# Kernel optimization log

Hardware: AMD Instinct MI355X
Metric: run time of the kernel (lower is better)

The kernel has to match this reference:

```python
import jax, jax.numpy as jnp
import numpy as np

THRESHOLD = 0.3
NEG_BIG = -2.0 ** 32  # matches tf -2**32 causal mask constant


def setup_inputs() -> dict:
    key = jax.random.key(0)
    kq, kt, kv = jax.random.split(key, 3)
    B, S, D = 16, 2048, 128
    Q = jax.random.normal(kq, (B, S, D), dtype=jnp.float32)
    T = jax.random.normal(kt, (B, S, D), dtype=jnp.float32)
    V = jax.random.normal(kv, (B, S, D), dtype=jnp.float32)
    return {"Q": Q, "T": T, "V": V}


def reference(Q, T, V):
    # scores: [B, S, S]
    A = jnp.einsum('bqd,bkd->bqk', Q, T)
    # Faithful to tf.where(A>thr, A, -2**32 * cast(A>thr)):
    # the false branch evaluates to 0 (mask is 0 there), NOT -2**32.
    A = jnp.where(A > THRESHOLD, A, jnp.zeros((), A.dtype))
    S = Q.shape[1]
    causal = jnp.triu(jnp.ones((S, S), dtype=bool), k=1)  # strictly upper = masked
    A = A + jnp.where(causal, jnp.asarray(NEG_BIG, A.dtype), jnp.zeros((), A.dtype))
    d_k = jnp.asarray(Q.shape[-1], A.dtype)
    A = A / jnp.sqrt(d_k)
    y = jax.nn.softmax(A, axis=-1)
    return jnp.einsum('bqk,bkd->bqd', y, V)
```

## Files before the change

kernel.cpp:

```cpp
#include <hip/hip_runtime.h>
#include <hip/hip_bf16.h>


#define S_LEN 2048
#define D_DIM 128
#define THRESH 0.3f
#define SCALE 0.08838834764831845f

typedef __bf16 bf16x8 __attribute__((ext_vector_type(8)));
typedef __bf16 bf16x4 __attribute__((ext_vector_type(4)));
typedef float f32x4 __attribute__((ext_vector_type(4)));

#define GLD16(g, l)                                                         \
    __builtin_amdgcn_global_load_lds(                                       \
        (const __attribute__((address_space(1))) unsigned int*)(g),         \
        (__attribute__((address_space(3))) unsigned int*)(l), 16, 0, 0)

__global__ void prep_kernel(const float* __restrict__ V, const float* __restrict__ T,
                            __bf16* __restrict__ Vt, __bf16* __restrict__ Tb) {
    __shared__ float tile[64][65];
    int bid = blockIdx.x;
    int tid = threadIdx.x;
    int b  = bid >> 6;
    int t2 = bid & 63;

    {
        int flat = tid * 16;
        int r = flat >> 7, cc = flat & 127;
        const float* p = T + ((size_t)b * S_LEN + t2 * 32 + r) * D_DIM + cc;
        __bf16* q = Tb + ((size_t)b * S_LEN + t2 * 32 + r) * D_DIM + cc;
        bf16x8 w0, w1;
        f32x4 a0 = *(const f32x4*)p,       a1 = *(const f32x4*)(p + 4);
        f32x4 a2 = *(const f32x4*)(p + 8), a3 = *(const f32x4*)(p + 12);
        #pragma unroll
        for (int j = 0; j < 4; ++j) {
            w0[j] = (__bf16)a0[j]; w0[4 + j] = (__bf16)a1[j];
            w1[j] = (__bf16)a2[j]; w1[4 + j] = (__bf16)a3[j];
        }
        *(bf16x8*)q = w0;
        *(bf16x8*)(q + 8) = w1;
    }

    int s0 = (t2 >> 1) * 64;
    int d0 = (t2 & 1) * 64;
    #pragma unroll
    for (int it = 0; it < 2; ++it) {
        int row = it * 32 + (tid >> 3);
        int c   = (tid & 7) * 8;
        const float* p = V + ((size_t)b * S_LEN + s0 + row) * D_DIM + d0 + c;
        *(f32x4*)(&tile[row][c])     = *(const f32x4*)p;
        *(f32x4*)(&tile[row][c + 4]) = *(const f32x4*)(p + 4);
    }
    __syncthreads();
    #pragma unroll
    for (int it = 0; it < 2; ++it) {
        int dr = it * 32 + (tid >> 3);
        int c  = (tid & 7) * 8;
        bf16x8 w;
        #pragma unroll
        for (int j = 0; j < 8; ++j) w[j] = (__bf16)tile[c + j][dr];
        *(bf16x8*)(Vt + ((size_t)b * D_DIM + d0 + dr) * S_LEN + s0 + c) = w;
    }
}

__global__ __launch_bounds__(256, 2)
void fa_kernel(const float* __restrict__ Q, const __bf16* __restrict__ Tb,
               const __bf16* __restrict__ Vt, float* __restrict__ O,
               float* __restrict__ pO, float* __restrict__ pL) {
    __shared__ __align__(16) unsigned char smem[73728];

    const int bid = blockIdx.x;
    const int b   = bid & 15;
    const int pi  = (bid >> 4) & 15;
    const int c   = bid >> 8;
    const int qtH = 31 - pi;
    const int L   = pi + 1;

    const int tid  = threadIdx.x;
    const int lane = tid & 63;
    const int wv   = tid >> 6;
    const int col  = lane & 15;
    const int quad = lane >> 4;

    unsigned char* Pb = smem + 65536;
    float* Lxf = (float*)(smem + 65536);

    const __bf16* TbB = Tb + (size_t)b * (S_LEN * D_DIM);
    const __bf16* VtB = Vt + (size_t)b * (D_DIM * S_LEN);

    int toff[4], voff[4];
    #pragma unroll
    for (int i = 0; i < 4; ++i) {
        int trw = wv * 16 + i * 4 + (lane >> 4);
        toff[i] = trw * 128 + (((lane & 15) ^ (trw & 7)) << 3);
        int drw = wv * 32 + i * 8 + (lane >> 3);
        voff[i] = drw * 2048 + (((lane & 7) ^ (drw & 7)) << 3);
    }

    auto issueTile = [&](int k0, int buf) {
        const __bf16* ts = TbB + (size_t)k0 * D_DIM;
        const __bf16* vs = VtB + k0;
        unsigned char* lt = smem + buf * 16384 + wv * 4096;
        unsigned char* lv = smem + 32768 + buf * 16384 + wv * 4096;
        #pragma unroll
        for (int i = 0; i < 4; ++i) GLD16(ts + toff[i], lt + i * 1024);
        #pragma unroll
        for (int i = 0; i < 4; ++i) GLD16(vs + voff[i], lv + i * 1024);
    };

    bf16x8 qf[4][4];
    auto loadQ = [&](int jq) {
        #pragma unroll
        for (int t = 0; t < 4; ++t) {
            const float* qptr = Q + ((size_t)b * S_LEN + jq * 64 + 16 * t + col) * D_DIM + quad * 8;
            #pragma unroll
            for (int kk = 0; kk < 4; ++kk) {
                f32x4 a = *(const f32x4*)(qptr + kk * 32);
                f32x4 d = *(const f32x4*)(qptr + kk * 32 + 4);
                #pragma unroll
                for (int j = 0; j < 4; ++j) { qf[t][kk][j] = (__bf16)a[j]; qf[t][kk][4 + j] = (__bf16)d[j]; }
            }
        }
    };

    f32x4 oacc[4][2];
    float lsum[4];
    float lfull[4][4];

    auto computeTile = [&](int buf, bool diag) {
        unsigned char* Tt = smem + buf * 16384;
        unsigned char* Vl = smem + 32768 + buf * 16384;

        f32x4 sacc[4];
        #pragma unroll
        for (int t = 0; t < 4; ++t) sacc[t] = {0.f, 0.f, 0.f, 0.f};
        __builtin_amdgcn_s_setprio(1);
        #pragma unroll
        for (int kk = 0; kk < 4; ++kk) {
            int trow = wv * 16 + col;
            bf16x8 tf = *(const bf16x8*)(Tt + trow * 256 + ((kk * 64 + quad * 16) ^ ((trow & 7) << 4)));
            #pragma unroll
            for (int t = 0; t < 4; ++t)
                sacc[t] = __builtin_amdgcn_mfma_f32_16x16x32_bf16(tf, qf[t][kk], sacc[t], 0, 0, 0);
        }
        __builtin_amdgcn_s_setprio(0);

        float p[4][4];
        #pragma unroll
        for (int t = 0; t < 4; ++t)
            #pragma unroll
            for (int r = 0; r < 4; ++r) {
                float s = sacc[t][r];
                float e = __expf(s * SCALE);
                p[t][r] = (s > THRESH) ? e : 1.0f;
            }
        if (diag) {
            #pragma unroll
            for (int t = 0; t < 4; ++t)
                #pragma unroll
                for (int r = 0; r < 4; ++r)
                    if (wv * 16 + quad * 4 + r > 16 * t + col) p[t][r] = 0.0f;
        }
        #pragma unroll
        for (int t = 0; t < 4; ++t)
            lsum[t] += (p[t][0] + p[t][1]) + (p[t][2] + p[t][3]);

        #pragma unroll
        for (int t = 0; t < 4; ++t) {
            int row = 16 * t + col;
            bf16x4 w = {(__bf16)p[t][0], (__bf16)p[t][1], (__bf16)p[t][2], (__bf16)p[t][3]};
            *(bf16x4*)(Pb + row * 128 + ((32 * wv + 8 * quad) ^ ((row & 7) << 4))) = w;
        }
        asm volatile("s_waitcnt lgkmcnt(0)" ::: "memory");
        __builtin_amdgcn_s_barrier();

        __builtin_amdgcn_s_setprio(1);
        #pragma unroll
        for (int kb = 0; kb < 2; ++kb) {
            bf16x8 pf[4];
            #pragma unroll
            for (int t = 0; t < 4; ++t) {
                int prow = 16 * t + col;
                pf[t] = *(const bf16x8*)(Pb + prow * 128 + ((kb * 64 + quad * 16) ^ ((prow & 7) << 4)));
            }
            #pragma unroll
            for (int dn = 0; dn < 2; ++dn) {
                int vrow = 32 * wv + 16 * dn + col;
                bf16x8 vf = *(const bf16x8*)(Vl + vrow * 128 + ((kb * 64 + quad * 16) ^ ((vrow & 7) << 4)));
                #pragma unroll
                for (int t = 0; t < 4; ++t)
                    oacc[t][dn] = __builtin_amdgcn_mfma_f32_16x16x32_bf16(pf[t], vf, oacc[t][dn], 0, 0, 0);
            }
        }
        __builtin_amdgcn_s_setprio(0);
    };

    auto runSeg = [&](int jq, int k0t, int nt) {
        loadQ(jq);
        #pragma unroll
        for (int t = 0; t < 4; ++t) {
            oacc[t][0] = {0.f, 0.f, 0.f, 0.f};
            oacc[t][1] = {0.f, 0.f, 0.f, 0.f};
            lsum[t] = 0.f;
        }
        issueTile(k0t * 64, 0);
        for (int s = 0; s < nt; ++s) {
            if (s + 1 < nt) {
                issueTile((k0t + s + 1) * 64, (s + 1) & 1);
                asm volatile("s_waitcnt vmcnt(8)" ::: "memory");
            } else {
                asm volatile("s_waitcnt vmcnt(0)" ::: "memory");
            }
            __builtin_amdgcn_s_barrier();
            computeTile(s & 1, k0t + s == jq);
            __builtin_amdgcn_s_barrier();
        }
    };

    auto finishSeg = [&]() {
        #pragma unroll
        for (int t = 0; t < 4; ++t) {
            float lw = lsum[t];
            lw += __shfl_xor(lw, 16);
            lw += __shfl_xor(lw, 32);
            if (quad == 0) Lxf[wv * 64 + 16 * t + col] = lw;
        }
        __syncthreads();
        #pragma unroll
        for (int t = 0; t < 4; ++t)
            #pragma unroll
            for (int r = 0; r < 4; ++r) {
                int q = 16 * t + quad * 4 + r;
                lfull[t][r] = (Lxf[q] + Lxf[64 + q]) + (Lxf[128 + q] + Lxf[192 + q]);
            }
        __syncthreads();
    };

    auto storeO = [&](int jq) {
        float* optr = O + ((size_t)b * S_LEN + jq * 64) * D_DIM;
        #pragma unroll
        for (int t = 0; t < 4; ++t)
            #pragma unroll
            for (int r = 0; r < 4; ++r) {
                float inv = 1.0f / lfull[t][r];
                #pragma unroll
                for (int dn = 0; dn < 2; ++dn)
                    optr[(16 * t + quad * 4 + r) * D_DIM + 32 * wv + 16 * dn + col] = oacc[t][dn][r] * inv;
            }
    };

    auto storePartial = [&]() {
        size_t slot = (size_t)((b * 16 + pi) * 2 + c);
        float* po = pO + slot * (64 * 128);
        float* pl = pL + slot * 64;
        #pragma unroll
        for (int t = 0; t < 4; ++t)
            #pragma unroll
            for (int r = 0; r < 4; ++r)
                #pragma unroll
                for (int dn = 0; dn < 2; ++dn)
                    po[(16 * t + quad * 4 + r) * 128 + 32 * wv + 16 * dn + col] = oacc[t][dn][r];
        if (wv == 0 && col == 0) {
            #pragma unroll
            for (int t = 0; t < 4; ++t)
                #pragma unroll
                for (int r = 0; r < 4; ++r)
                    pl[16 * t + quad * 4 + r] = lfull[t][r];
        }
    };

    if (c == 0) {
        runSeg(pi, 0, L);
        finishSeg();
        storeO(pi);
        runSeg(qtH, 0, 17 - L);
        finishSeg();
        storePartial();
    } else {
        runSeg(qtH, 17 - L, 16);
        finishSeg();
        storePartial();
    }
}

__global__ void nrm_kernel(const float* __restrict__ pO, const float* __restrict__ pL,
                           float* __restrict__ O) {
    int gid  = blockIdx.x * 256 + threadIdx.x;
    int flat = gid * 16;
    int pr   = flat >> 13;
    int rl   = (flat >> 7) & 63;
    int cc   = flat & 127;
    int b = pr >> 4, pi = pr & 15;
    const float* p0 = pO + ((size_t)pr * 2)     * 8192 + rl * 128 + cc;
    const float* p1 = pO + ((size_t)pr * 2 + 1) * 8192 + rl * 128 + cc;
    float inv = 1.0f / (pL[(pr * 2) * 64 + rl] + pL[(pr * 2 + 1) * 64 + rl]);
    float* op = O + ((size_t)b * S_LEN + (31 - pi) * 64 + rl) * D_DIM + cc;
    #pragma unroll
    for (int j = 0; j < 4; ++j) {
        f32x4 a = *(const f32x4*)(p0 + j * 4);
        f32x4 d = *(const f32x4*)(p1 + j * 4);
        f32x4 o;
        #pragma unroll
        for (int r = 0; r < 4; ++r) o[r] = (a[r] + d[r]) * inv;
        *(f32x4*)(op + j * 4) = o;
    }
}

extern "C" void kernel_launch(void* const* d_in, const int* in_sizes, int n_in,
                              void* d_out, int out_size, void* d_ws, size_t ws_size,
                              hipStream_t stream) {
    const float* Q = (const float*)d_in[0];
    const float* T = (const float*)d_in[1];
    const float* V = (const float*)d_in[2];
    float* O = (float*)d_out;

    unsigned char* ws = (unsigned char*)d_ws;
    __bf16* Vt = (__bf16*)ws;
    __bf16* Tb = (__bf16*)(ws + 8388608);
    float*  pO = (float*)(ws + 16777216);
    float*  pL = (float*)(ws + 16777216 + 16777216);

    prep_kernel<<<1024, 256, 0, stream>>>(V, T, Vt, Tb);
    fa_kernel<<<512, 256, 0, stream>>>(Q, Tb, Vt, O, pO, pL);
    nrm_kernel<<<512, 256, 0, stream>>>(pO, pL, O);
}
```

Baseline: 131.4 us.

## Widen attention blocks to 128 query rows, triple-buffer K/V, fuse partial merge

The attention kernel now uses 512-thread blocks covering 128 query rows, with two wave halves sharing each K/V tile, so every loaded tile is reused by twice as many queries. It adds a three-stage K/V buffer ring and double-buffered P storage, which lets prefetch run two tiles ahead and drops the trailing barrier. The separate normalization kernel is removed: the second chunk's block spin-waits on an atomic flag, adds the first chunk's partial output and sum, and writes the final result. This cuts one launch and some global traffic, but it relies on co-residency for the spin-wait, uses more LDS per block, and halves the grid size.

```diff
diff --git a/kernel.cpp b/kernel.cpp
--- a/kernel.cpp
+++ b/kernel.cpp
@@ -17,10 +17,12 @@
         (__attribute__((address_space(3))) unsigned int*)(l), 16, 0, 0)
 
 __global__ void prep_kernel(const float* __restrict__ V, const float* __restrict__ T,
-                            __bf16* __restrict__ Vt, __bf16* __restrict__ Tb) {
+                            __bf16* __restrict__ Vt, __bf16* __restrict__ Tb,
+                            int* __restrict__ done) {
     __shared__ float tile[64][65];
     int bid = blockIdx.x;
     int tid = threadIdx.x;
+    if (bid == 0 && tid < 128) done[tid] = 0;
     int b  = bid >> 6;
     int t2 = bid & 63;
 
@@ -63,56 +65,59 @@
     }
 }
 
-__global__ __launch_bounds__(256, 2)
+__global__ __launch_bounds__(512, 2)
 void fa_kernel(const float* __restrict__ Q, const __bf16* __restrict__ Tb,
                const __bf16* __restrict__ Vt, float* __restrict__ O,
-               float* __restrict__ pO, float* __restrict__ pL) {
-    __shared__ __align__(16) unsigned char smem[73728];
+               float* __restrict__ pO, float* __restrict__ pL,
+               int* __restrict__ done) {
+    __shared__ __align__(16) unsigned char smem[131072];
 
     const int bid = blockIdx.x;
     const int b   = bid & 15;
-    const int pi  = (bid >> 4) & 15;
-    const int c   = bid >> 8;
-    const int qtH = 31 - pi;
-    const int L   = pi + 1;
+    const int pi  = (bid >> 4) & 7;
+    const int c   = bid >> 7;
+    const int Lt  = 2 * pi + 2;
+    const int pr  = b * 8 + pi;
+    const int jqL = pi, jqH = 15 - pi;
 
     const int tid  = threadIdx.x;
     const int lane = tid & 63;
     const int wv   = tid >> 6;
     const int col  = lane & 15;
     const int quad = lane >> 4;
-
-    unsigned char* Pb = smem + 65536;
-    float* Lxf = (float*)(smem + 65536);
+    const int kg   = wv & 3;
+    const int h    = wv >> 2;
+
+    float* Lxf = (float*)(smem + 98304);
 
     const __bf16* TbB = Tb + (size_t)b * (S_LEN * D_DIM);
     const __bf16* VtB = Vt + (size_t)b * (D_DIM * S_LEN);
 
-    int toff[4], voff[4];
+    int toff[2], voff[2];
     #pragma unroll
-    for (int i = 0; i < 4; ++i) {
-        int trw = wv * 16 + i * 4 + (lane >> 4);
+    for (int i = 0; i < 2; ++i) {
+        int trw = wv * 8 + i * 4 + quad;
         toff[i] = trw * 128 + (((lane & 15) ^ (trw & 7)) << 3);
-        int drw = wv * 32 + i * 8 + (lane >> 3);
+        int drw = wv * 16 + i * 8 + (lane >> 3);
         voff[i] = drw * 2048 + (((lane & 7) ^ (drw & 7)) << 3);
     }
 
     auto issueTile = [&](int k0, int buf) {
         const __bf16* ts = TbB + (size_t)k0 * D_DIM;
         const __bf16* vs = VtB + k0;
-        unsigned char* lt = smem + buf * 16384 + wv * 4096;
-        unsigned char* lv = smem + 32768 + buf * 16384 + wv * 4096;
-        #pragma unroll
-        for (int i = 0; i < 4; ++i) GLD16(ts + toff[i], lt + i * 1024);
-        #pragma unroll
-        for (int i = 0; i < 4; ++i) GLD16(vs + voff[i], lv + i * 1024);
+        unsigned char* lt = smem + buf * 16384 + wv * 2048;
+        unsigned char* lv = smem + 49152 + buf * 16384 + wv * 2048;
+        GLD16(ts + toff[0], lt);
+        GLD16(ts + toff[1], lt + 1024);
+        GLD16(vs + voff[0], lv);
+        GLD16(vs + voff[1], lv + 1024);
     };
 
     bf16x8 qf[4][4];
     auto loadQ = [&](int jq) {
         #pragma unroll
         for (int t = 0; t < 4; ++t) {
-            const float* qptr = Q + ((size_t)b * S_LEN + jq * 64 + 16 * t + col) * D_DIM + quad * 8;
+            const float* qptr = Q + ((size_t)b * S_LEN + jq * 128 + h * 64 + 16 * t + col) * D_DIM + quad * 8;
             #pragma unroll
             for (int kk = 0; kk < 4; ++kk) {
                 f32x4 a = *(const f32x4*)(qptr + kk * 32);
@@ -127,17 +132,14 @@
     float lsum[4];
     float lfull[4][4];
 
-    auto computeTile = [&](int buf, bool diag) {
-        unsigned char* Tt = smem + buf * 16384;
-        unsigned char* Vl = smem + 32768 + buf * 16384;
-
+    auto computeTile = [&](unsigned char* Tt, unsigned char* Vl, unsigned char* Pb, int dKt) {
         f32x4 sacc[4];
         #pragma unroll
         for (int t = 0; t < 4; ++t) sacc[t] = {0.f, 0.f, 0.f, 0.f};
         __builtin_amdgcn_s_setprio(1);
         #pragma unroll
         for (int kk = 0; kk < 4; ++kk) {
-            int trow = wv * 16 + col;
+            int trow = kg * 16 + col;
             bf16x8 tf = *(const bf16x8*)(Tt + trow * 256 + ((kk * 64 + quad * 16) ^ ((trow & 7) << 4)));
             #pragma unroll
             for (int t = 0; t < 4; ++t)
@@ -154,12 +156,12 @@
                 float e = __expf(s * SCALE);
                 p[t][r] = (s > THRESH) ? e : 1.0f;
             }
-        if (diag) {
+        if (dKt < 64) {
             #pragma unroll
             for (int t = 0; t < 4; ++t)
                 #pragma unroll
                 for (int r = 0; r < 4; ++r)
-                    if (wv * 16 + quad * 4 + r > 16 * t + col) p[t][r] = 0.0f;
+                    if (kg * 16 + quad * 4 + r - (h * 64 + 16 * t + col) > dKt) p[t][r] = 0.0f;
         }
         #pragma unroll
         for (int t = 0; t < 4; ++t)
@@ -167,9 +169,9 @@
 
         #pragma unroll
         for (int t = 0; t < 4; ++t) {
-            int row = 16 * t + col;
+            int row = h * 64 + 16 * t + col;
             bf16x4 w = {(__bf16)p[t][0], (__bf16)p[t][1], (__bf16)p[t][2], (__bf16)p[t][3]};
-            *(bf16x4*)(Pb + row * 128 + ((32 * wv + 8 * quad) ^ ((row & 7) << 4))) = w;
+            *(bf16x4*)(Pb + row * 128 + ((kg * 32 + quad * 8) ^ ((row & 7) << 4))) = w;
         }
         asm volatile("s_waitcnt lgkmcnt(0)" ::: "memory");
         __builtin_amdgcn_s_barrier();
@@ -180,12 +182,12 @@
             bf16x8 pf[4];
             #pragma unroll
             for (int t = 0; t < 4; ++t) {
-                int prow = 16 * t + col;
+                int prow = h * 64 + 16 * t + col;
                 pf[t] = *(const bf16x8*)(Pb + prow * 128 + ((kb * 64 + quad * 16) ^ ((prow & 7) << 4)));
             }
             #pragma unroll
             for (int dn = 0; dn < 2; ++dn) {
-                int vrow = 32 * wv + 16 * dn + col;
+                int vrow = kg * 32 + 16 * dn + col;
                 bf16x8 vf = *(const bf16x8*)(Vl + vrow * 128 + ((kb * 64 + quad * 16) ^ ((vrow & 7) << 4)));
                 #pragma unroll
                 for (int t = 0; t < 4; ++t)
@@ -204,20 +206,27 @@
             lsum[t] = 0.f;
         }
         issueTile(k0t * 64, 0);
+        if (nt > 1) issueTile((k0t + 1) * 64, 1);
+        int cb = 0;
         for (int s = 0; s < nt; ++s) {
             if (s + 1 < nt) {
-                issueTile((k0t + s + 1) * 64, (s + 1) & 1);
-                asm volatile("s_waitcnt vmcnt(8)" ::: "memory");
+                asm volatile("s_waitcnt vmcnt(4)" ::: "memory");
             } else {
                 asm volatile("s_waitcnt vmcnt(0)" ::: "memory");
             }
             __builtin_amdgcn_s_barrier();
-            computeTile(s & 1, k0t + s == jq);
-            __builtin_amdgcn_s_barrier();
+            if (s + 2 < nt) {
+                int nb = cb + 2; if (nb >= 3) nb -= 3;
+                issueTile((k0t + s + 2) * 64, nb);
+            }
+            computeTile(smem + cb * 16384, smem + 49152 + cb * 16384,
+                        smem + 98304 + (s & 1) * 16384, 128 * jq - 64 * (k0t + s));
+            cb = (cb == 2) ? 0 : cb + 1;
         }
     };
 
     auto finishSeg = [&]() {
+        __syncthreads();
         #pragma unroll
         for (int t = 0; t < 4; ++t) {
             float lw = lsum[t];
@@ -230,14 +239,15 @@
         for (int t = 0; t < 4; ++t)
             #pragma unroll
             for (int r = 0; r < 4; ++r) {
-                int q = 16 * t + quad * 4 + r;
-                lfull[t][r] = (Lxf[q] + Lxf[64 + q]) + (Lxf[128 + q] + Lxf[192 + q]);
+                int q16 = 16 * t + quad * 4 + r;
+                lfull[t][r] = (Lxf[(4 * h + 0) * 64 + q16] + Lxf[(4 * h + 1) * 64 + q16]) +
+                              (Lxf[(4 * h + 2) * 64 + q16] + Lxf[(4 * h + 3) * 64 + q16]);
             }
         __syncthreads();
     };
 
     auto storeO = [&](int jq) {
-        float* optr = O + ((size_t)b * S_LEN + jq * 64) * D_DIM;
+        float* optr = O + ((size_t)b * S_LEN + jq * 128 + h * 64) * D_DIM + kg * 32;
         #pragma unroll
         for (int t = 0; t < 4; ++t)
             #pragma unroll
@@ -245,64 +255,65 @@
                 float inv = 1.0f / lfull[t][r];
                 #pragma unroll
                 for (int dn = 0; dn < 2; ++dn)
-                    optr[(16 * t + quad * 4 + r) * D_DIM + 32 * wv + 16 * dn + col] = oacc[t][dn][r] * inv;
+                    optr[(16 * t + quad * 4 + r) * D_DIM + 16 * dn + col] = oacc[t][dn][r] * inv;
             }
     };
 
     auto storePartial = [&]() {
-        size_t slot = (size_t)((b * 16 + pi) * 2 + c);
-        float* po = pO + slot * (64 * 128);
-        float* pl = pL + slot * 64;
+        float* po = pO + (size_t)pr * (128 * 128);
+        float* pl = pL + (size_t)pr * 128;
         #pragma unroll
         for (int t = 0; t < 4; ++t)
             #pragma unroll
             for (int r = 0; r < 4; ++r)
                 #pragma unroll
                 for (int dn = 0; dn < 2; ++dn)
-                    po[(16 * t + quad * 4 + r) * 128 + 32 * wv + 16 * dn + col] = oacc[t][dn][r];
-        if (wv == 0 && col == 0) {
+                    po[(h * 64 + 16 * t + quad * 4 + r) * 128 + kg * 32 + 16 * dn + col] = oacc[t][dn][r];
+        if (kg == 0 && col == 0) {
             #pragma unroll
             for (int t = 0; t < 4; ++t)
                 #pragma unroll
                 for (int r = 0; r < 4; ++r)
-                    pl[16 * t + quad * 4 + r] = lfull[t][r];
-        }
+                    pl[h * 64 + 16 * t + quad * 4 + r] = lfull[t][r];
+        }
+        __threadfence();
+        __syncthreads();
+        if (tid == 0)
+            __hip_atomic_fetch_add(&done[pr], 1, __ATOMIC_RELEASE, __HIP_MEMORY_SCOPE_AGENT);
+    };
+
+    auto addPartial = [&]() {
+        if (tid == 0) {
+            while (__hip_atomic_load(&done[pr], __ATOMIC_ACQUIRE, __HIP_MEMORY_SCOPE_AGENT) < 1)
+                __builtin_amdgcn_s_sleep(8);
+        }
+        __syncthreads();
+        __threadfence();
+        const float* po = pO + (size_t)pr * (128 * 128);
+        const float* pl = pL + (size_t)pr * 128;
+        #pragma unroll
+        for (int t = 0; t < 4; ++t)
+            #pragma unroll
+            for (int r = 0; r < 4; ++r) {
+                #pragma unroll
+                for (int dn = 0; dn < 2; ++dn)
+                    oacc[t][dn][r] += po[(h * 64 + 16 * t + quad * 4 + r) * 128 + kg * 32 + 16 * dn + col];
+                lfull[t][r] += pl[h * 64 + 16 * t + quad * 4 + r];
+            }
     };
 
     if (c == 0) {
-        runSeg(pi, 0, L);
+        runSeg(jqL, 0, Lt);
         finishSeg();
-        storeO(pi);
-        runSeg(qtH, 0, 17 - L);
+        storeO(jqL);
+        runSeg(jqH, 0, 17 - Lt);
         finishSeg();
         storePartial();
     } else {
-        runSeg(qtH, 17 - L, 16);
+        runSeg(jqH, 17 - Lt, 17);
         finishSeg();
-        storePartial();
-    }
-}
-
-__global__ void nrm_kernel(const float* __restrict__ pO, const float* __restrict__ pL,
-                           float* __restrict__ O) {
-    int gid  = blockIdx.x * 256 + threadIdx.x;
-    int flat = gid * 16;
-    int pr   = flat >> 13;
-    int rl   = (flat >> 7) & 63;
-    int cc   = flat & 127;
-    int b = pr >> 4, pi = pr & 15;
-    const float* p0 = pO + ((size_t)pr * 2)     * 8192 + rl * 128 + cc;
-    const float* p1 = pO + ((size_t)pr * 2 + 1) * 8192 + rl * 128 + cc;
-    float inv = 1.0f / (pL[(pr * 2) * 64 + rl] + pL[(pr * 2 + 1) * 64 + rl]);
-    float* op = O + ((size_t)b * S_LEN + (31 - pi) * 64 + rl) * D_DIM + cc;
-    #pragma unroll
-    for (int j = 0; j < 4; ++j) {
-        f32x4 a = *(const f32x4*)(p0 + j * 4);
-        f32x4 d = *(const f32x4*)(p1 + j * 4);
-        f32x4 o;
-        #pragma unroll
-        for (int r = 0; r < 4; ++r) o[r] = (a[r] + d[r]) * inv;
-        *(f32x4*)(op + j * 4) = o;
+        addPartial();
+        storeO(jqH);
     }
 }
 
@@ -318,9 +329,9 @@
     __bf16* Vt = (__bf16*)ws;
     __bf16* Tb = (__bf16*)(ws + 8388608);
     float*  pO = (float*)(ws + 16777216);
-    float*  pL = (float*)(ws + 16777216 + 16777216);
-
-    prep_kernel<<<1024, 256, 0, stream>>>(V, T, Vt, Tb);
-    fa_kernel<<<512, 256, 0, stream>>>(Q, Tb, Vt, O, pO, pL);
-    nrm_kernel<<<512, 256, 0, stream>>>(pO, pL, O);
+    float*  pL = (float*)(ws + 16777216 + 8388608);
+    int*  done = (int*)(ws + 16777216 + 8388608 + 65536);
+
+    prep_kernel<<<1024, 256, 0, stream>>>(V, T, Vt, Tb, done);
+    fa_kernel<<<256, 512, 0, stream>>>(Q, Tb, Vt, O, pO, pL, done);
 }
```

Result: slower. 204.2 us (+55.4%).

## Split causal work across four KV chunks per block pair, single-buffer LDS, bf16 partials

Applied to the files above, without the earlier changes.

Each block now takes one of four fixed KV-range chunks over the concatenated low and high query-tile pair, instead of two halves. This doubles the grid to 1024 blocks, giving finer-grained load balancing and more parallelism. LDS drops from double to single buffering, shrinking shared memory so more blocks can be resident, at the cost of no longer overlapping tile loads with compute. Partial outputs are stored as bf16 and reduced over up to five slots in a rewritten normalize kernel. This cuts partial traffic but adds rounding error and more reduction work.

```diff
diff --git a/kernel.cpp b/kernel.cpp
--- a/kernel.cpp
+++ b/kernel.cpp
@@ -66,15 +66,16 @@
 __global__ __launch_bounds__(256, 2)
 void fa_kernel(const float* __restrict__ Q, const __bf16* __restrict__ Tb,
                const __bf16* __restrict__ Vt, float* __restrict__ O,
-               float* __restrict__ pO, float* __restrict__ pL) {
-    __shared__ __align__(16) unsigned char smem[73728];
+               __bf16* __restrict__ pO, float* __restrict__ pL) {
+    __shared__ __align__(16) unsigned char smem[40960];
 
     const int bid = blockIdx.x;
     const int b   = bid & 15;
     const int pi  = (bid >> 4) & 15;
     const int c   = bid >> 8;
-    const int qtH = 31 - pi;
-    const int L   = pi + 1;
+    const int Lt  = pi + 1;
+    const int pr  = b * 16 + pi;
+    const int jqL = pi, jqH = 31 - pi;
 
     const int tid  = threadIdx.x;
     const int lane = tid & 63;
@@ -82,8 +83,8 @@
     const int col  = lane & 15;
     const int quad = lane >> 4;
 
-    unsigned char* Pb = smem + 65536;
-    float* Lxf = (float*)(smem + 65536);
+    unsigned char* Pb = smem + 32768;
+    float* Lxf = (float*)(smem + 32768);
 
     const __bf16* TbB = Tb + (size_t)b * (S_LEN * D_DIM);
     const __bf16* VtB = Vt + (size_t)b * (D_DIM * S_LEN);
@@ -97,11 +98,11 @@
         voff[i] = drw * 2048 + (((lane & 7) ^ (drw & 7)) << 3);
     }
 
-    auto issueTile = [&](int k0, int buf) {
+    auto issueTile = [&](int k0) {
         const __bf16* ts = TbB + (size_t)k0 * D_DIM;
         const __bf16* vs = VtB + k0;
-        unsigned char* lt = smem + buf * 16384 + wv * 4096;
-        unsigned char* lv = smem + 32768 + buf * 16384 + wv * 4096;
+        unsigned char* lt = smem + wv * 4096;
+        unsigned char* lv = smem + 16384 + wv * 4096;
         #pragma unroll
         for (int i = 0; i < 4; ++i) GLD16(ts + toff[i], lt + i * 1024);
         #pragma unroll
@@ -127,9 +128,9 @@
     float lsum[4];
     float lfull[4][4];
 
-    auto computeTile = [&](int buf, bool diag) {
-        unsigned char* Tt = smem + buf * 16384;
-        unsigned char* Vl = smem + 32768 + buf * 16384;
+    auto computeTile = [&](bool diag) {
+        unsigned char* Tt = smem;
+        unsigned char* Vl = smem + 16384;
 
         f32x4 sacc[4];
         #pragma unroll
@@ -203,17 +204,13 @@
             oacc[t][1] = {0.f, 0.f, 0.f, 0.f};
             lsum[t] = 0.f;
         }
-        issueTile(k0t * 64, 0);
+        issueTile(k0t * 64);
         for (int s = 0; s < nt; ++s) {
-            if (s + 1 < nt) {
-                issueTile((k0t + s + 1) * 64, (s + 1) & 1);
-                asm volatile("s_waitcnt vmcnt(8)" ::: "memory");
-            } else {
-                asm volatile("s_waitcnt vmcnt(0)" ::: "memory");
-            }
+            asm volatile("s_waitcnt vmcnt(0)" ::: "memory");
             __builtin_amdgcn_s_barrier();
-            computeTile(s & 1, k0t + s == jq);
+            computeTile(k0t + s == jq);
             __builtin_amdgcn_s_barrier();
+            if (s + 1 < nt) issueTile((k0t + s + 1) * 64);
         }
     };
 
@@ -249,17 +246,16 @@
             }
     };
 
-    auto storePartial = [&]() {
-        size_t slot = (size_t)((b * 16 + pi) * 2 + c);
-        float* po = pO + slot * (64 * 128);
-        float* pl = pL + slot * 64;
+    auto storePartial = [&](int slot) {
+        __bf16* po = pO + (size_t)(pr * 5 + slot) * (64 * 128);
+        float*  pl = pL + (size_t)(pr * 5 + slot) * 64;
         #pragma unroll
         for (int t = 0; t < 4; ++t)
             #pragma unroll
             for (int r = 0; r < 4; ++r)
                 #pragma unroll
                 for (int dn = 0; dn < 2; ++dn)
-                    po[(16 * t + quad * 4 + r) * 128 + 32 * wv + 16 * dn + col] = oacc[t][dn][r];
+                    po[(16 * t + quad * 4 + r) * 128 + 32 * wv + 16 * dn + col] = (__bf16)oacc[t][dn][r];
         if (wv == 0 && col == 0) {
             #pragma unroll
             for (int t = 0; t < 4; ++t)
@@ -269,39 +265,68 @@
         }
     };
 
-    if (c == 0) {
-        runSeg(pi, 0, L);
+    const int Btab[5] = {0, 9, 17, 25, 33};
+    const int lo = Btab[c], hi = Btab[c + 1];
+
+    int lend = Lt < hi ? Lt : hi;
+    if (lo < lend) {
+        runSeg(jqL, lo, lend - lo);
         finishSeg();
-        storeO(pi);
-        runSeg(qtH, 0, 17 - L);
+        if (Lt <= 9)      storeO(jqL);
+        else if (c == 0)  storePartial(0);
+        else              storePartial(4);
+    }
+    int hstart = Lt > lo ? Lt : lo;
+    if (hstart < hi) {
+        runSeg(jqH, hstart - Lt, hi - hstart);
         finishSeg();
-        storePartial();
+        storePartial(c);
+    }
+}
+
+__global__ void nrm_kernel(const __bf16* __restrict__ pO, const float* __restrict__ pL,
+                           float* __restrict__ O) {
+    int bid  = blockIdx.x;
+    int half = bid & 1;
+    int tile = (bid >> 1) & 1;
+    int pi   = (bid >> 2) & 15;
+    int b    = bid >> 6;
+    int Lt   = pi + 1;
+    int tid  = threadIdx.x;
+    int row  = half * 32 + (tid >> 3);
+    int cc   = (tid & 7) * 16;
+    int pr   = b * 16 + pi;
+
+    float acc[16];
+    #pragma unroll
+    for (int j = 0; j < 16; ++j) acc[j] = 0.f;
+    float l = 0.f;
+
+    auto addSlot = [&](int slot) {
+        const __bf16* po = pO + (size_t)(pr * 5 + slot) * (64 * 128) + row * 128 + cc;
+        bf16x8 a = *(const bf16x8*)po;
+        bf16x8 d = *(const bf16x8*)(po + 8);
+        #pragma unroll
+        for (int j = 0; j < 8; ++j) { acc[j] += (float)a[j]; acc[8 + j] += (float)d[j]; }
+        l += pL[(pr * 5 + slot) * 64 + row];
+    };
+
+    int qt;
+    if (tile == 1) {
+        qt = 31 - pi;
+        for (int s = (Lt < 9) ? 0 : 1; s < 4; ++s) addSlot(s);
     } else {
-        runSeg(qtH, 17 - L, 16);
-        finishSeg();
-        storePartial();
-    }
-}
-
-__global__ void nrm_kernel(const float* __restrict__ pO, const float* __restrict__ pL,
-                           float* __restrict__ O) {
-    int gid  = blockIdx.x * 256 + threadIdx.x;
-    int flat = gid * 16;
-    int pr   = flat >> 13;
-    int rl   = (flat >> 7) & 63;
-    int cc   = flat & 127;
-    int b = pr >> 4, pi = pr & 15;
-    const float* p0 = pO + ((size_t)pr * 2)     * 8192 + rl * 128 + cc;
-    const float* p1 = pO + ((size_t)pr * 2 + 1) * 8192 + rl * 128 + cc;
-    float inv = 1.0f / (pL[(pr * 2) * 64 + rl] + pL[(pr * 2 + 1) * 64 + rl]);
-    float* op = O + ((size_t)b * S_LEN + (31 - pi) * 64 + rl) * D_DIM + cc;
+        if (Lt <= 9) return;
+        qt = pi;
+        addSlot(0); addSlot(4);
+    }
+    float inv = 1.0f / l;
+    float* op = O + ((size_t)b * S_LEN + qt * 64 + row) * D_DIM + cc;
     #pragma unroll
     for (int j = 0; j < 4; ++j) {
-        f32x4 a = *(const f32x4*)(p0 + j * 4);
-        f32x4 d = *(const f32x4*)(p1 + j * 4);
         f32x4 o;
         #pragma unroll
-        for (int r = 0; r < 4; ++r) o[r] = (a[r] + d[r]) * inv;
+        for (int r = 0; r < 4; ++r) o[r] = acc[j * 4 + r] * inv;
         *(f32x4*)(op + j * 4) = o;
     }
 }
@@ -317,10 +342,10 @@
     unsigned char* ws = (unsigned char*)d_ws;
     __bf16* Vt = (__bf16*)ws;
     __bf16* Tb = (__bf16*)(ws + 8388608);
-    float*  pO = (float*)(ws + 16777216);
-    float*  pL = (float*)(ws + 16777216 + 16777216);
+    __bf16* pO = (__bf16*)(ws + 16777216);
+    float*  pL = (float*)(ws + 16777216 + 20971520);
 
     prep_kernel<<<1024, 256, 0, stream>>>(V, T, Vt, Tb);
-    fa_kernel<<<512, 256, 0, stream>>>(Q, Tb, Vt, O, pO, pL);
-    nrm_kernel<<<512, 256, 0, stream>>>(pO, pL, O);
+    fa_kernel<<<1024, 256, 0, stream>>>(Q, Tb, Vt, O, pO, pL);
+    nrm_kernel<<<1024, 256, 0, stream>>>(pO, pL, O);
 }
```

Result: slower. 144.7 us (+10.2%).

## Merge split-K partial reduction into attention kernel via atomic flag handoff

Applied to the files above, without the earlier changes.

Removes the separate normalization kernel. The block handling the second half of a query tile now spins on an atomic completion flag, adds the other block's partial output (stored as bf16 instead of fp32) and writes the final result. The tile split is rebalanced so the c==0 block skips the partial entirely when L reaches 16. The pipelined loop now waits fully on loads before issuing the next tile and drops the trailing barrier, and exp is computed with exp2f on a prescaled constant. This saves a kernel launch and pO traffic, but it relies on all blocks being co-resident to avoid deadlock, adds bf16 rounding of partials, and may reduce load/compute overlap.

```diff
diff --git a/kernel.cpp b/kernel.cpp
--- a/kernel.cpp
+++ b/kernel.cpp
@@ -5,7 +5,7 @@
 #define S_LEN 2048
 #define D_DIM 128
 #define THRESH 0.3f
-#define SCALE 0.08838834764831845f
+#define EXP2C 0.12751742f
 
 typedef __bf16 bf16x8 __attribute__((ext_vector_type(8)));
 typedef __bf16 bf16x4 __attribute__((ext_vector_type(4)));
@@ -17,10 +17,12 @@
         (__attribute__((address_space(3))) unsigned int*)(l), 16, 0, 0)
 
 __global__ void prep_kernel(const float* __restrict__ V, const float* __restrict__ T,
-                            __bf16* __restrict__ Vt, __bf16* __restrict__ Tb) {
+                            __bf16* __restrict__ Vt, __bf16* __restrict__ Tb,
+                            int* __restrict__ done) {
     __shared__ float tile[64][65];
     int bid = blockIdx.x;
     int tid = threadIdx.x;
+    if (bid == 0) done[tid] = 0;
     int b  = bid >> 6;
     int t2 = bid & 63;
 
@@ -66,7 +68,8 @@
 __global__ __launch_bounds__(256, 2)
 void fa_kernel(const float* __restrict__ Q, const __bf16* __restrict__ Tb,
                const __bf16* __restrict__ Vt, float* __restrict__ O,
-               float* __restrict__ pO, float* __restrict__ pL) {
+               __bf16* __restrict__ pO, float* __restrict__ pL,
+               int* __restrict__ done) {
     __shared__ __align__(16) unsigned char smem[73728];
 
     const int bid = blockIdx.x;
@@ -75,6 +78,7 @@
     const int c   = bid >> 8;
     const int qtH = 31 - pi;
     const int L   = pi + 1;
+    const int pr  = b * 16 + pi;
 
     const int tid  = threadIdx.x;
     const int lane = tid & 63;
@@ -151,7 +155,7 @@
             #pragma unroll
             for (int r = 0; r < 4; ++r) {
                 float s = sacc[t][r];
-                float e = __expf(s * SCALE);
+                float e = exp2f(s * EXP2C);
                 p[t][r] = (s > THRESH) ? e : 1.0f;
             }
         if (diag) {
@@ -205,19 +209,15 @@
         }
         issueTile(k0t * 64, 0);
         for (int s = 0; s < nt; ++s) {
-            if (s + 1 < nt) {
-                issueTile((k0t + s + 1) * 64, (s + 1) & 1);
-                asm volatile("s_waitcnt vmcnt(8)" ::: "memory");
-            } else {
-                asm volatile("s_waitcnt vmcnt(0)" ::: "memory");
-            }
+            asm volatile("s_waitcnt vmcnt(0)" ::: "memory");
             __builtin_amdgcn_s_barrier();
+            if (s + 1 < nt) issueTile((k0t + s + 1) * 64, (s + 1) & 1);
             computeTile(s & 1, k0t + s == jq);
-            __builtin_amdgcn_s_barrier();
         }
     };
 
     auto finishSeg = [&]() {
+        __syncthreads();
         #pragma unroll
         for (int t = 0; t < 4; ++t) {
             float lw = lsum[t];
@@ -250,16 +250,15 @@
     };
 
     auto storePartial = [&]() {
-        size_t slot = (size_t)((b * 16 + pi) * 2 + c);
-        float* po = pO + slot * (64 * 128);
-        float* pl = pL + slot * 64;
+        __bf16* po = pO + (size_t)pr * (64 * 128);
+        float*  pl = pL + (size_t)pr * 64;
         #pragma unroll
         for (int t = 0; t < 4; ++t)
             #pragma unroll
             for (int r = 0; r < 4; ++r)
                 #pragma unroll
                 for (int dn = 0; dn < 2; ++dn)
-                    po[(16 * t + quad * 4 + r) * 128 + 32 * wv + 16 * dn + col] = oacc[t][dn][r];
+                    po[(16 * t + quad * 4 + r) * 128 + 32 * wv + 16 * dn + col] = (__bf16)oacc[t][dn][r];
         if (wv == 0 && col == 0) {
             #pragma unroll
             for (int t = 0; t < 4; ++t)
@@ -267,42 +266,46 @@
                 for (int r = 0; r < 4; ++r)
                     pl[16 * t + quad * 4 + r] = lfull[t][r];
         }
+        __threadfence();
+        __syncthreads();
+        if (tid == 0)
+            __hip_atomic_fetch_add(&done[pr], 1, __ATOMIC_RELEASE, __HIP_MEMORY_SCOPE_AGENT);
+    };
+
+    auto addPartial = [&]() {
+        if (tid == 0) {
+            while (__hip_atomic_load(&done[pr], __ATOMIC_ACQUIRE, __HIP_MEMORY_SCOPE_AGENT) < 1)
+                __builtin_amdgcn_s_sleep(8);
+        }
+        __syncthreads();
+        __threadfence();
+        const __bf16* po = pO + (size_t)pr * (64 * 128);
+        const float*  pl = pL + (size_t)pr * 64;
+        #pragma unroll
+        for (int t = 0; t < 4; ++t)
+            #pragma unroll
+            for (int r = 0; r < 4; ++r) {
+                #pragma unroll
+                for (int dn = 0; dn < 2; ++dn)
+                    oacc[t][dn][r] += (float)po[(16 * t + quad * 4 + r) * 128 + 32 * wv + 16 * dn + col];
+                lfull[t][r] += pl[16 * t + quad * 4 + r];
+            }
     };
 
     if (c == 0) {
         runSeg(pi, 0, L);
         finishSeg();
         storeO(pi);
-        runSeg(qtH, 0, 17 - L);
+        if (L < 16) {
+            runSeg(qtH, 0, 16 - L);
+            finishSeg();
+            storePartial();
+        }
+    } else {
+        runSeg(qtH, 16 - L, 17);
         finishSeg();
-        storePartial();
-    } else {
-        runSeg(qtH, 17 - L, 16);
-        finishSeg();
-        storePartial();
-    }
-}
-
-__global__ void nrm_kernel(const float* __restrict__ pO, const float* __restrict__ pL,
-                           float* __restrict__ O) {
-    int gid  = blockIdx.x * 256 + threadIdx.x;
-    int flat = gid * 16;
-    int pr   = flat >> 13;
-    int rl   = (flat >> 7) & 63;
-    int cc   = flat & 127;
-    int b = pr >> 4, pi = pr & 15;
-    const float* p0 = pO + ((size_t)pr * 2)     * 8192 + rl * 128 + cc;
-    const float* p1 = pO + ((size_t)pr * 2 + 1) * 8192 + rl * 128 + cc;
-    float inv = 1.0f / (pL[(pr * 2) * 64 + rl] + pL[(pr * 2 + 1) * 64 + rl]);
-    float* op = O + ((size_t)b * S_LEN + (31 - pi) * 64 + rl) * D_DIM + cc;
-    #pragma unroll
-    for (int j = 0; j < 4; ++j) {
-        f32x4 a = *(const f32x4*)(p0 + j * 4);
-        f32x4 d = *(const f32x4*)(p1 + j * 4);
-        f32x4 o;
-        #pragma unroll
-        for (int r = 0; r < 4; ++r) o[r] = (a[r] + d[r]) * inv;
-        *(f32x4*)(op + j * 4) = o;
+        if (L < 16) addPartial();
+        storeO(qtH);
     }
 }
 
@@ -317,10 +320,10 @@
     unsigned char* ws = (unsigned char*)d_ws;
     __bf16* Vt = (__bf16*)ws;
     __bf16* Tb = (__bf16*)(ws + 8388608);
-    float*  pO = (float*)(ws + 16777216);
-    float*  pL = (float*)(ws + 16777216 + 16777216);
-
-    prep_kernel<<<1024, 256, 0, stream>>>(V, T, Vt, Tb);
-    fa_kernel<<<512, 256, 0, stream>>>(Q, Tb, Vt, O, pO, pL);
-    nrm_kernel<<<512, 256, 0, stream>>>(pO, pL, O);
+    __bf16* pO = (__bf16*)(ws + 16777216);
+    float*  pL = (float*)(ws + 16777216 + 4194304);
+    int*  done = (int*)(ws + 16777216 + 4194304 + 65536);
+
+    prep_kernel<<<1024, 256, 0, stream>>>(V, T, Vt, Tb, done);
+    fa_kernel<<<512, 256, 0, stream>>>(Q, Tb, Vt, O, pO, pL, done);
 }
```

Result: slower. 181.5 us (+38.1%).
